# Performance work log

Hardware: AMD Instinct MI355X
Metric: run time of the kernel (lower is better)

Reference implementation:

```python
import jax, jax.numpy as jnp
import numpy as np

W_R = 25.0  # regularization weight (init kwarg w_r)


def _quat_multiply(q1, q2):
    # q1, q2: [..., 4] broadcastable, (w, x, y, z)
    w1, x1, y1, z1 = q1[..., 0], q1[..., 1], q1[..., 2], q1[..., 3]
    w2, x2, y2, z2 = q2[..., 0], q2[..., 1], q2[..., 2], q2[..., 3]
    w = w1 * w2 - x1 * x2 - y1 * y2 - z1 * z2
    x = w1 * x2 + x1 * w2 + y1 * z2 - z1 * y2
    y = w1 * y2 - x1 * z2 + y1 * w2 + z1 * x2
    z = w1 * z2 + x1 * y2 - y1 * x2 + z1 * w2
    return jnp.stack([w, x, y, z], axis=-1)


def _closest_point_mean_dist(tp, grid, grid_min, grid_max):
    # tp: [P, N, 3] transformed points; grid: [R, R, R, 3]
    R = grid.shape[0]
    normalized = (tp - grid_min) / (grid_max - grid_min)
    idx = jnp.clip(jnp.round(normalized * (R - 1)), 0, R - 1).astype(jnp.int32)
    cp = grid[idx[..., 0], idx[..., 1], idx[..., 2]]  # [P, N, 3] gather
    dist = jnp.linalg.norm(tp - cp, axis=-1)          # [P, N]
    return jnp.sum(jnp.mean(dist, axis=-1))           # sum over planes/axes of per-point mean


def _forward(pred_planes, pred_axes, surface_points, closest_point_grid, grid_min, grid_max):
    planes = pred_planes[0]  # [3, 4]
    axes = pred_axes[0]      # [3, 4]
    pts = surface_points     # [N, 3]

    # --- reflection loss (vectorized over 3 planes) ---
    n = planes[:, :3]                               # [3, 3]
    d = planes[:, 3]                                # [3]
    proj = jnp.einsum('nc,pc->pn', pts, n) + d[:, None]          # [3, N]
    reflected = pts[None] - 2.0 * proj[..., None] * n[:, None, :]  # [3, N, 3]
    loss_plane = _closest_point_mean_dist(reflected, closest_point_grid, grid_min, grid_max)

    # --- rotation loss (vectorized over 3 quaternions) ---
    pts_quat = jnp.pad(pts, ((0, 0), (1, 0)))        # [N, 4], w = 0
    q = axes                                         # [3, 4]
    q_conj = q * jnp.array([1.0, -1.0, -1.0, -1.0], dtype=q.dtype)
    rotated = _quat_multiply(_quat_multiply(q[:, None, :], pts_quat[None]), q_conj[:, None, :])[..., 1:]  # [3, N, 3]
    loss_axis = _closest_point_mean_dist(rotated, closest_point_grid, grid_min, grid_max)

    total_loss_sd = loss_plane + loss_axis

    # --- regularization ---
    eye = jnp.eye(3, dtype=pts.dtype)
    A = n @ n.T - eye
    v = axes[:, 1:]
    v = v / jnp.maximum(jnp.linalg.norm(v, axis=1, keepdims=True), 1e-12)
    B = v @ v.T - eye
    total_loss_r = jnp.sum(A ** 2) + jnp.sum(B ** 2)

    final_loss = total_loss_sd + W_R * total_loss_r
    return final_loss, total_loss_sd, total_loss_r


def setup_inputs() -> dict:
    key = jax.random.key(0)
    k1, k2, k3, k4 = jax.random.split(key, 4)
    N, R = 1_000_000, 256
    return {
        'pred_planes': jax.random.normal(k1, (1, 3, 4), dtype=jnp.float32),
        'pred_axes': jax.random.normal(k2, (1, 3, 4), dtype=jnp.float32),
        'surface_points': jax.random.uniform(k3, (N, 3), dtype=jnp.float32),
        'closest_point_grid': jax.random.uniform(k4, (R, R, R, 3), dtype=jnp.float32),
        'grid_min': jnp.zeros((3,), dtype=jnp.float32),
        'grid_max': jnp.ones((3,), dtype=jnp.float32),
    }


def reference(pred_planes, pred_axes, surface_points, closest_point_grid, grid_min, grid_max):
    return _forward(pred_planes, pred_axes, surface_points, closest_point_grid, grid_min, grid_max)
```

## Files before the change

### kernel.cpp

```cpp
#include <hip/hip_runtime.h>
#include <math.h>


#define RGRID 256
#define PTS_PER_THREAD 4

__global__ void __launch_bounds__(256)
symloss_main(const float* __restrict__ planes, const float* __restrict__ axes,
             const float* __restrict__ pts, const float* __restrict__ grid,
             const float* __restrict__ gmin, const float* __restrict__ gmax,
             float* __restrict__ acc, int N) {
    float P[12], Q[12];
#pragma unroll
    for (int i = 0; i < 12; ++i) { P[i] = planes[i]; Q[i] = axes[i]; }
    const float g0 = gmin[0], g1 = gmin[1], g2 = gmin[2];
    const float s0 = 255.0f / (gmax[0] - g0);
    const float s1 = 255.0f / (gmax[1] - g1);
    const float s2 = 255.0f / (gmax[2] - g2);

    const int t  = blockIdx.x * blockDim.x + threadIdx.x;
    const int p0 = t * PTS_PER_THREAD;

    float lsum = 0.0f;
    if (p0 < N) {
        float px[4], py[4], pz[4];
        int npts;
        if (p0 + 3 < N) {
            const float4* pts4 = (const float4*)pts;
            float4 a = pts4[3 * t + 0];
            float4 b = pts4[3 * t + 1];
            float4 c = pts4[3 * t + 2];
            px[0] = a.x; py[0] = a.y; pz[0] = a.z;
            px[1] = a.w; py[1] = b.x; pz[1] = b.y;
            px[2] = b.z; py[2] = b.w; pz[2] = c.x;
            px[3] = c.y; py[3] = c.z; pz[3] = c.w;
            npts = 4;
        } else {
            npts = N - p0;
#pragma unroll
            for (int i = 0; i < 4; ++i) {
                int p = p0 + (i < npts ? i : 0);
                px[i] = pts[3 * p + 0];
                py[i] = pts[3 * p + 1];
                pz[i] = pts[3 * p + 2];
            }
        }

        float tx[24], ty[24], tz[24];
#pragma unroll
        for (int i = 0; i < 4; ++i) {
#pragma unroll
            for (int k = 0; k < 3; ++k) {
                float nx = P[4 * k + 0], ny = P[4 * k + 1], nz = P[4 * k + 2], d = P[4 * k + 3];
                float proj = px[i] * nx + py[i] * ny + pz[i] * nz + d;
                float m2p = -2.0f * proj;
                int o = i * 6 + k;
                tx[o] = fmaf(m2p, nx, px[i]);
                ty[o] = fmaf(m2p, ny, py[i]);
                tz[o] = fmaf(m2p, nz, pz[i]);
            }
#pragma unroll
            for (int k = 0; k < 3; ++k) {
                float qw = Q[4 * k + 0], qx = Q[4 * k + 1], qy = Q[4 * k + 2], qz = Q[4 * k + 3];
                float rw = -(qx * px[i] + qy * py[i] + qz * pz[i]);
                float rx = qw * px[i] + qy * pz[i] - qz * py[i];
                float ry = qw * py[i] - qx * pz[i] + qz * px[i];
                float rz = qw * pz[i] + qx * py[i] - qy * px[i];
                int o = i * 6 + 3 + k;
                tx[o] = -rw * qx + rx * qw - ry * qz + rz * qy;
                ty[o] = -rw * qy + rx * qz + ry * qw - rz * qx;
                tz[o] = -rw * qz - rx * qy + ry * qx + rz * qw;
            }
        }

        int base[24];
#pragma unroll
        for (int o = 0; o < 24; ++o) {
            float f0 = rintf((tx[o] - g0) * s0);
            float f1 = rintf((ty[o] - g1) * s1);
            float f2 = rintf((tz[o] - g2) * s2);
            f0 = fminf(fmaxf(f0, 0.0f), 255.0f);
            f1 = fminf(fmaxf(f1, 0.0f), 255.0f);
            f2 = fminf(fmaxf(f2, 0.0f), 255.0f);
            int i0 = (int)f0, i1 = (int)f1, i2 = (int)f2;
            base[o] = ((i0 * RGRID + i1) * RGRID + i2) * 3;
        }
        float partial[4] = {0.0f, 0.0f, 0.0f, 0.0f};
#pragma unroll
        for (int o = 0; o < 24; ++o) {
            float cx = grid[base[o] + 0];
            float cy = grid[base[o] + 1];
            float cz = grid[base[o] + 2];
            float dx = tx[o] - cx, dy = ty[o] - cy, dz = tz[o] - cz;
            partial[o / 6] += sqrtf(fmaf(dx, dx, fmaf(dy, dy, dz * dz)));
        }
#pragma unroll
        for (int i = 0; i < 4; ++i)
            if (i < npts) lsum += partial[i];
    }

#pragma unroll
    for (int off = 32; off > 0; off >>= 1)
        lsum += __shfl_down(lsum, off, 64);
    __shared__ float wsum[4];
    int lane = threadIdx.x & 63;
    int wid  = threadIdx.x >> 6;
    if (lane == 0) wsum[wid] = lsum;
    __syncthreads();
    if (threadIdx.x == 0) {
        atomicAdd(acc, wsum[0] + wsum[1] + wsum[2] + wsum[3]);
    }
}

__global__ void symloss_final(const float* __restrict__ planes,
                              const float* __restrict__ axes,
                              const float* __restrict__ acc,
                              float* __restrict__ out, float invN) {
    float sd = acc[0] * invN;

    float n[3][3];
#pragma unroll
    for (int i = 0; i < 3; ++i)
#pragma unroll
        for (int j = 0; j < 3; ++j) n[i][j] = planes[4 * i + j];

    float sA = 0.0f;
#pragma unroll
    for (int i = 0; i < 3; ++i)
#pragma unroll
        for (int j = 0; j < 3; ++j) {
            float a = n[i][0] * n[j][0] + n[i][1] * n[j][1] + n[i][2] * n[j][2]
                      - (i == j ? 1.0f : 0.0f);
            sA += a * a;
        }

    float v[3][3];
#pragma unroll
    for (int i = 0; i < 3; ++i) {
        float vx = axes[4 * i + 1], vy = axes[4 * i + 2], vz = axes[4 * i + 3];
        float nrm = sqrtf(vx * vx + vy * vy + vz * vz);
        nrm = fmaxf(nrm, 1e-12f);
        v[i][0] = vx / nrm; v[i][1] = vy / nrm; v[i][2] = vz / nrm;
    }
    float sB = 0.0f;
#pragma unroll
    for (int i = 0; i < 3; ++i)
#pragma unroll
        for (int j = 0; j < 3; ++j) {
            float b = v[i][0] * v[j][0] + v[i][1] * v[j][1] + v[i][2] * v[j][2]
                      - (i == j ? 1.0f : 0.0f);
            sB += b * b;
        }

    float r = sA + sB;
    out[0] = sd + 25.0f * r;
    out[1] = sd;
    out[2] = r;
}

extern "C" void kernel_launch(void* const* d_in, const int* in_sizes, int n_in,
                              void* d_out, int out_size, void* d_ws, size_t ws_size,
                              hipStream_t stream) {
    const float* planes = (const float*)d_in[0];
    const float* axes   = (const float*)d_in[1];
    const float* pts    = (const float*)d_in[2];
    const float* grid   = (const float*)d_in[3];
    const float* gmin   = (const float*)d_in[4];
    const float* gmax   = (const float*)d_in[5];
    float* out = (float*)d_out;
    float* acc = (float*)d_ws;

    int N = in_sizes[2] / 3;

    hipMemsetAsync(acc, 0, sizeof(float), stream);

    int nthreads = (N + PTS_PER_THREAD - 1) / PTS_PER_THREAD;
    int blocks = (nthreads + 255) / 256;
    hipLaunchKernelGGL(symloss_main, dim3(blocks), dim3(256), 0, stream,
                       planes, axes, pts, grid, gmin, gmax, acc, N);
    hipLaunchKernelGGL(symloss_final, dim3(1), dim3(1), 0, stream,
                       planes, axes, acc, out, 1.0f / (float)N);
}
```

Before: 266.3 us.

## Fuse final reduction into main kernel and split gathers into two register-light halves

Removes the separate single-thread finalization kernel by having the last block, detected through an atomic ticket counter, compute the regularization and write the outputs. The 24 transformed points per thread are processed in two halves of 12 (planes, then quaternions), with all gathers of each half issued before use, cutting register pressure. A min-blocks launch bound of 4 is added to push occupancy. Fewer gathers in flight per thread and possible spills from the launch bound are the risks.

```diff
diff --git a/kernel.cpp b/kernel.cpp
--- a/kernel.cpp
+++ b/kernel.cpp
@@ -5,11 +5,11 @@
 #define RGRID 256
 #define PTS_PER_THREAD 4
 
-__global__ void __launch_bounds__(256)
+__global__ void __launch_bounds__(256, 4)
 symloss_main(const float* __restrict__ planes, const float* __restrict__ axes,
              const float* __restrict__ pts, const float* __restrict__ grid,
              const float* __restrict__ gmin, const float* __restrict__ gmax,
-             float* __restrict__ acc, int N) {
+             float* __restrict__ acc, float* __restrict__ out, int N) {
     float P[12], Q[12];
 #pragma unroll
     for (int i = 0; i < 12; ++i) { P[i] = planes[i]; Q[i] = axes[i]; }
@@ -46,54 +46,63 @@
             }
         }
 
-        float tx[24], ty[24], tz[24];
+        float partial[4] = {0.0f, 0.0f, 0.0f, 0.0f};
+
 #pragma unroll
-        for (int i = 0; i < 4; ++i) {
+        for (int h = 0; h < 2; ++h) {
+            float tx[12], ty[12], tz[12];
 #pragma unroll
-            for (int k = 0; k < 3; ++k) {
-                float nx = P[4 * k + 0], ny = P[4 * k + 1], nz = P[4 * k + 2], d = P[4 * k + 3];
-                float proj = px[i] * nx + py[i] * ny + pz[i] * nz + d;
-                float m2p = -2.0f * proj;
-                int o = i * 6 + k;
-                tx[o] = fmaf(m2p, nx, px[i]);
-                ty[o] = fmaf(m2p, ny, py[i]);
-                tz[o] = fmaf(m2p, nz, pz[i]);
+            for (int i = 0; i < 4; ++i) {
+#pragma unroll
+                for (int k = 0; k < 3; ++k) {
+                    const int o = i * 3 + k;
+                    if (h == 0) {
+                        float nx = P[4 * k + 0], ny = P[4 * k + 1], nz = P[4 * k + 2], d = P[4 * k + 3];
+                        float proj = px[i] * nx + py[i] * ny + pz[i] * nz + d;
+                        float m2p = -2.0f * proj;
+                        tx[o] = fmaf(m2p, nx, px[i]);
+                        ty[o] = fmaf(m2p, ny, py[i]);
+                        tz[o] = fmaf(m2p, nz, pz[i]);
+                    } else {
+                        float qw = Q[4 * k + 0], qx = Q[4 * k + 1], qy = Q[4 * k + 2], qz = Q[4 * k + 3];
+                        float rw = -(qx * px[i] + qy * py[i] + qz * pz[i]);
+                        float rx = qw * px[i] + qy * pz[i] - qz * py[i];
+                        float ry = qw * py[i] - qx * pz[i] + qz * px[i];
+                        float rz = qw * pz[i] + qx * py[i] - qy * px[i];
+                        tx[o] = -rw * qx + rx * qw - ry * qz + rz * qy;
+                        ty[o] = -rw * qy + rx * qz + ry * qw - rz * qx;
+                        tz[o] = -rw * qz - rx * qy + ry * qx + rz * qw;
+                    }
+                }
+            }
+
+            int base[12];
+#pragma unroll
+            for (int o = 0; o < 12; ++o) {
+                float f0 = rintf((tx[o] - g0) * s0);
+                float f1 = rintf((ty[o] - g1) * s1);
+                float f2 = rintf((tz[o] - g2) * s2);
+                f0 = fminf(fmaxf(f0, 0.0f), 255.0f);
+                f1 = fminf(fmaxf(f1, 0.0f), 255.0f);
+                f2 = fminf(fmaxf(f2, 0.0f), 255.0f);
+                int i0 = (int)f0, i1 = (int)f1, i2 = (int)f2;
+                base[o] = ((i0 * RGRID + i1) * RGRID + i2) * 3;
+            }
+
+            float cx[12], cy[12], cz[12];
+#pragma unroll
+            for (int o = 0; o < 12; ++o) {
+                cx[o] = grid[base[o] + 0];
+                cy[o] = grid[base[o] + 1];
+                cz[o] = grid[base[o] + 2];
             }
 #pragma unroll
-            for (int k = 0; k < 3; ++k) {
-                float qw = Q[4 * k + 0], qx = Q[4 * k + 1], qy = Q[4 * k + 2], qz = Q[4 * k + 3];
-                float rw = -(qx * px[i] + qy * py[i] + qz * pz[i]);
-                float rx = qw * px[i] + qy * pz[i] - qz * py[i];
-                float ry = qw * py[i] - qx * pz[i] + qz * px[i];
-                float rz = qw * pz[i] + qx * py[i] - qy * px[i];
-                int o = i * 6 + 3 + k;
-                tx[o] = -rw * qx + rx * qw - ry * qz + rz * qy;
-                ty[o] = -rw * qy + rx * qz + ry * qw - rz * qx;
-                tz[o] = -rw * qz - rx * qy + ry * qx + rz * qw;
+            for (int o = 0; o < 12; ++o) {
+                float dx = tx[o] - cx[o], dy = ty[o] - cy[o], dz = tz[o] - cz[o];
+                partial[o / 3] += sqrtf(fmaf(dx, dx, fmaf(dy, dy, dz * dz)));
             }
         }
 
-        int base[24];
-#pragma unroll
-        for (int o = 0; o < 24; ++o) {
-            float f0 = rintf((tx[o] - g0) * s0);
-            float f1 = rintf((ty[o] - g1) * s1);
-            float f2 = rintf((tz[o] - g2) * s2);
-            f0 = fminf(fmaxf(f0, 0.0f), 255.0f);
-            f1 = fminf(fmaxf(f1, 0.0f), 255.0f);
-            f2 = fminf(fmaxf(f2, 0.0f), 255.0f);
-            int i0 = (int)f0, i1 = (int)f1, i2 = (int)f2;
-            base[o] = ((i0 * RGRID + i1) * RGRID + i2) * 3;
-        }
-        float partial[4] = {0.0f, 0.0f, 0.0f, 0.0f};
-#pragma unroll
-        for (int o = 0; o < 24; ++o) {
-            float cx = grid[base[o] + 0];
-            float cy = grid[base[o] + 1];
-            float cz = grid[base[o] + 2];
-            float dx = tx[o] - cx, dy = ty[o] - cy, dz = tz[o] - cz;
-            partial[o / 6] += sqrtf(fmaf(dx, dx, fmaf(dy, dy, dz * dz)));
-        }
 #pragma unroll
         for (int i = 0; i < 4; ++i)
             if (i < npts) lsum += partial[i];
@@ -107,55 +116,48 @@
     int wid  = threadIdx.x >> 6;
     if (lane == 0) wsum[wid] = lsum;
     __syncthreads();
+
     if (threadIdx.x == 0) {
         atomicAdd(acc, wsum[0] + wsum[1] + wsum[2] + wsum[3]);
+        __threadfence();
+        unsigned prev = atomicAdd((unsigned*)(acc + 1), 1u);
+        if (prev == gridDim.x - 1) {
+            float total = atomicAdd(acc, 0.0f);
+            float sd = total / (float)N;
+
+            float sA = 0.0f;
+#pragma unroll
+            for (int i = 0; i < 3; ++i)
+#pragma unroll
+                for (int j = 0; j < 3; ++j) {
+                    float a = P[4 * i + 0] * P[4 * j + 0] + P[4 * i + 1] * P[4 * j + 1]
+                            + P[4 * i + 2] * P[4 * j + 2] - (i == j ? 1.0f : 0.0f);
+                    sA += a * a;
+                }
+            float v[3][3];
+#pragma unroll
+            for (int i = 0; i < 3; ++i) {
+                float vx = Q[4 * i + 1], vy = Q[4 * i + 2], vz = Q[4 * i + 3];
+                float nrm = sqrtf(vx * vx + vy * vy + vz * vz);
+                nrm = fmaxf(nrm, 1e-12f);
+                v[i][0] = vx / nrm; v[i][1] = vy / nrm; v[i][2] = vz / nrm;
+            }
+            float sB = 0.0f;
+#pragma unroll
+            for (int i = 0; i < 3; ++i)
+#pragma unroll
+                for (int j = 0; j < 3; ++j) {
+                    float b = v[i][0] * v[j][0] + v[i][1] * v[j][1] + v[i][2] * v[j][2]
+                            - (i == j ? 1.0f : 0.0f);
+                    sB += b * b;
+                }
+
+            float r = sA + sB;
+            out[0] = sd + 25.0f * r;
+            out[1] = sd;
+            out[2] = r;
+        }
     }
-}
-
-__global__ void symloss_final(const float* __restrict__ planes,
-                              const float* __restrict__ axes,
-                              const float* __restrict__ acc,
-                              float* __restrict__ out, float invN) {
-    float sd = acc[0] * invN;
-
-    float n[3][3];
-#pragma unroll
-    for (int i = 0; i < 3; ++i)
-#pragma unroll
-        for (int j = 0; j < 3; ++j) n[i][j] = planes[4 * i + j];
-
-    float sA = 0.0f;
-#pragma unroll
-    for (int i = 0; i < 3; ++i)
-#pragma unroll
-        for (int j = 0; j < 3; ++j) {
-            float a = n[i][0] * n[j][0] + n[i][1] * n[j][1] + n[i][2] * n[j][2]
-                      - (i == j ? 1.0f : 0.0f);
-            sA += a * a;
-        }
-
-    float v[3][3];
-#pragma unroll
-    for (int i = 0; i < 3; ++i) {
-        float vx = axes[4 * i + 1], vy = axes[4 * i + 2], vz = axes[4 * i + 3];
-        float nrm = sqrtf(vx * vx + vy * vy + vz * vz);
-        nrm = fmaxf(nrm, 1e-12f);
-        v[i][0] = vx / nrm; v[i][1] = vy / nrm; v[i][2] = vz / nrm;
-    }
-    float sB = 0.0f;
-#pragma unroll
-    for (int i = 0; i < 3; ++i)
-#pragma unroll
-        for (int j = 0; j < 3; ++j) {
-            float b = v[i][0] * v[j][0] + v[i][1] * v[j][1] + v[i][2] * v[j][2]
-                      - (i == j ? 1.0f : 0.0f);
-            sB += b * b;
-        }
-
-    float r = sA + sB;
-    out[0] = sd + 25.0f * r;
-    out[1] = sd;
-    out[2] = r;
 }
 
 extern "C" void kernel_launch(void* const* d_in, const int* in_sizes, int n_in,
@@ -172,12 +174,10 @@
 
     int N = in_sizes[2] / 3;
 
-    hipMemsetAsync(acc, 0, sizeof(float), stream);
+    hipMemsetAsync(acc, 0, 2 * sizeof(float), stream);
 
     int nthreads = (N + PTS_PER_THREAD - 1) / PTS_PER_THREAD;
     int blocks = (nthreads + 255) / 256;
     hipLaunchKernelGGL(symloss_main, dim3(blocks), dim3(256), 0, stream,
-                       planes, axes, pts, grid, gmin, gmax, acc, N);
-    hipLaunchKernelGGL(symloss_final, dim3(1), dim3(1), 0, stream,
-                       planes, axes, acc, out, 1.0f / (float)N);
+                       planes, axes, pts, grid, gmin, gmax, acc, out, N);
 }
```

Result: slower. 294.7 us (+10.7%).
